# Kernel tuning notes

Measured on AMD Instinct MI355X. Metric: run time of the kernel, lower is better.

## Reference

```python
import jax, jax.numpy as jnp
import numpy as np

ENC, DEC, B, S = 1024, 1024, 32, 2048


def setup_inputs() -> dict:
    key = jax.random.key(0)
    k1, k2, k3, k4, k5, k6 = jax.random.split(key, 6)
    scale_attn = 1.0 / np.sqrt(ENC + DEC)
    return {
        "decoder_hidden": jax.random.normal(k1, (B, DEC), dtype=jnp.float32),
        "encoder_outputs": jax.random.normal(k2, (B, S, ENC), dtype=jnp.float32),
        "mask": jax.random.randint(k3, (B, S), 0, 2, dtype=jnp.int32),
        "W_attn": jax.random.normal(k4, (ENC + DEC, DEC), dtype=jnp.float32) * scale_attn,
        "b_attn": jax.random.normal(k5, (DEC,), dtype=jnp.float32) * 0.02,
        "v_w": jax.random.normal(k6, (DEC,), dtype=jnp.float32) * (1.0 / np.sqrt(DEC)),
    }


def reference(decoder_hidden, encoder_outputs, mask, W_attn, b_attn, v_w):
    # Split cat((dec_exp, enc)) @ W into two GEMMs (same math, no repeat/concat).
    dec_dim = decoder_hidden.shape[-1]
    W_dec = W_attn[:dec_dim]      # [DEC, DEC]
    W_enc = W_attn[dec_dim:]      # [ENC, DEC]
    dec_proj = decoder_hidden @ W_dec                      # [B, DEC]
    enc_proj = jnp.einsum("bse,ed->bsd", encoder_outputs, W_enc)  # [B, S, DEC]
    energy = jnp.tanh(dec_proj[:, None, :] + enc_proj + b_attn)   # [B, S, DEC]
    scores = jnp.einsum("bsd,d->bs", energy, v_w)                 # [B, S]
    scores = jnp.where(mask == 0, -1e9, scores)
    attn_weights = jax.nn.softmax(scores, axis=1)                 # [B, S]
    context = jnp.einsum("bs,bse->be", attn_weights, encoder_outputs)  # [B, ENC]
    return (context, attn_weights)
```

## Files before the change

### kernel.cpp

```cpp
#include <hip/hip_runtime.h>
#include <hip/hip_bf16.h>
#include <cstdint>


#define ENCD 1024
#define DECD 1024
#define BATCH 32
#define SEQ 2048
#define MTOT (BATCH * SEQ)
#define KDIM 1024
#define NDIM 1024

typedef __attribute__((ext_vector_type(4))) float f32x4;
typedef __attribute__((ext_vector_type(8))) __bf16 bf16x8;
typedef __attribute__((ext_vector_type(8))) unsigned short u16x8;

__device__ __forceinline__ unsigned short f2bf(float f) {
  unsigned int u = __builtin_bit_cast(unsigned int, f);
  u += 0x7fffu + ((u >> 16) & 1u);
  return (unsigned short)(u >> 16);
}

__device__ __forceinline__ float bf2f(unsigned short h) {
  return __builtin_bit_cast(float, (unsigned int)h << 16);
}

__device__ __forceinline__ void async_lds16(const unsigned short* g, unsigned short* l) {
  __builtin_amdgcn_global_load_lds(
      (const __attribute__((address_space(1))) unsigned int*)g,
      (__attribute__((address_space(3))) unsigned int*)l, 16, 0, 0);
}

__device__ __forceinline__ void barx() {
  __builtin_amdgcn_s_barrier();
  asm volatile("" ::: "memory");
}

template <int N>
__device__ __forceinline__ void waitv() {
  if constexpr (N == 0) {
    asm volatile("s_waitcnt vmcnt(0)" ::: "memory");
  } else {
    asm volatile("s_waitcnt vmcnt(8)" ::: "memory");
  }
}

__global__ void conv_bf16_k(const float* __restrict__ src, unsigned short* __restrict__ dst) {
  const long i = ((long)blockIdx.x * 256 + threadIdx.x) * 8;
  const f32x4 f0 = *(const f32x4*)(src + i);
  const f32x4 f1 = *(const f32x4*)(src + i + 4);
  u16x8 v;
  v[0] = f2bf(f0[0]); v[1] = f2bf(f0[1]); v[2] = f2bf(f0[2]); v[3] = f2bf(f0[3]);
  v[4] = f2bf(f1[0]); v[5] = f2bf(f1[1]); v[6] = f2bf(f1[2]); v[7] = f2bf(f1[3]);
  *(u16x8*)(dst + i) = v;
}

__global__ void wt_k(const float* __restrict__ W, unsigned short* __restrict__ Wt) {
  __shared__ unsigned short t[64][65];
  const int k0 = blockIdx.x * 64, n0 = blockIdx.y * 64;
  const int tx = threadIdx.x & 63, ty = threadIdx.x >> 6;
#pragma unroll
  for (int i = 0; i < 16; ++i) {
    const int k = ty + i * 4;
    t[k][tx] = f2bf(W[(long)(DECD + k0 + k) * NDIM + n0 + tx]);
  }
  __syncthreads();
#pragma unroll
  for (int i = 0; i < 16; ++i) {
    const int n = ty + i * 4;
    Wt[(long)(n0 + n) * KDIM + k0 + tx] = t[tx][n];
  }
}

__global__ __launch_bounds__(256) void prep_k(
    const float* __restrict__ dec, const float* __restrict__ enc,
    const float* __restrict__ W, const float* __restrict__ bias,
    float* __restrict__ dp, unsigned short* __restrict__ Wt,
    unsigned short* __restrict__ Abf) {
  const int gb = blockIdx.x;
  const int tid = threadIdx.x;
  if (gb < 128) {
    const int b = gb >> 2;
    const int n = (gb & 3) * 256 + tid;
    const float* d = dec + b * DECD;
    const float* w = W + n;
    float acc = bias[n];
#pragma unroll 8
    for (int k = 0; k < 1024; ++k) acc = fmaf(d[k], w[(size_t)k * NDIM], acc);
    dp[b * NDIM + n] = acc;
  } else if (gb < 384) {
    __shared__ unsigned short t[64][65];
    const int g2 = gb - 128;
    const int k0 = (g2 & 15) * 64, n0 = (g2 >> 4) * 64;
    const int tx = tid & 63, ty = tid >> 6;
#pragma unroll
    for (int i = 0; i < 16; ++i) {
      const int k = ty + i * 4;
      t[k][tx] = f2bf(W[(size_t)(DECD + k0 + k) * NDIM + n0 + tx]);
    }
    __syncthreads();
#pragma unroll
    for (int i = 0; i < 16; ++i) {
      const int n = ty + i * 4;
      Wt[(size_t)(n0 + n) * KDIM + k0 + tx] = t[tx][n];
    }
  } else {
    const long i = ((long)(gb - 384) * 256 + tid) * 8;
    const f32x4 f0 = *(const f32x4*)(enc + i);
    const f32x4 f1 = *(const f32x4*)(enc + i + 4);
    u16x8 v;
    v[0] = f2bf(f0[0]); v[1] = f2bf(f0[1]); v[2] = f2bf(f0[2]); v[3] = f2bf(f0[3]);
    v[4] = f2bf(f1[0]); v[5] = f2bf(f1[1]); v[6] = f2bf(f1[2]); v[7] = f2bf(f1[3]);
    *(u16x8*)(Abf + i) = v;
  }
}


__device__ __forceinline__ void stage4(const unsigned short* gbase, unsigned short* lbase,
                                       int wv, int srow, int schunk, int k0) {
#pragma unroll
  for (int j = 0; j < 4; ++j) {
    async_lds16(gbase + (size_t)(j * 64 + wv * 8 + srow) * KDIM + k0 + schunk * 8,
                lbase + (j * 64 + wv * 8) * 64);
  }
}

template <bool STG, int BW>
__device__ __forceinline__ void gtile2(
    unsigned short* sAc, unsigned short* sBc,
    const unsigned short* Ab, const unsigned short* Bb, int k2,
    int wm, int wn, int wv, int quad, int l15, int srow, int schunk,
    f32x4 (&acc)[8][4], bf16x8 (&aF)[4][2], bf16x8 (&bF)[4][2]) {
  const int sw = l15 & 7;
#define RDF(buf, row, h) \
  __builtin_bit_cast(bf16x8, *(const u16x8*)&(buf)[(row) * 64 + ((((h) * 4 + quad) ^ sw) * 8)])
#pragma unroll
  for (int mt = 0; mt < 4; ++mt) {
    const int row = wm * 128 + mt * 16 + l15;
    aF[mt][0] = RDF(sAc, row, 0);
    aF[mt][1] = RDF(sAc, row, 1);
  }
#pragma unroll
  for (int nt = 0; nt < 2; ++nt) {
    const int row = wn * 64 + nt * 16 + l15;
    bF[nt][0] = RDF(sBc, row, 0);
    bF[nt][1] = RDF(sBc, row, 1);
  }
  barx();
  __builtin_amdgcn_s_setprio(1);
#pragma unroll
  for (int h = 0; h < 2; ++h)
#pragma unroll
    for (int mt = 0; mt < 4; ++mt)
#pragma unroll
      for (int nt = 0; nt < 2; ++nt)
        acc[mt][nt] = __builtin_amdgcn_mfma_f32_16x16x32_bf16(aF[mt][h], bF[nt][h], acc[mt][nt], 0, 0, 0);
  __builtin_amdgcn_s_setprio(0);
  barx();
#pragma unroll
  for (int nt = 2; nt < 4; ++nt) {
    const int row = wn * 64 + nt * 16 + l15;
    bF[nt][0] = RDF(sBc, row, 0);
    bF[nt][1] = RDF(sBc, row, 1);
  }
  barx();
  __builtin_amdgcn_s_setprio(1);
#pragma unroll
  for (int h = 0; h < 2; ++h)
#pragma unroll
    for (int mt = 0; mt < 4; ++mt)
#pragma unroll
      for (int nt = 0; nt < 2; ++nt)
        acc[mt][2 + nt] = __builtin_amdgcn_mfma_f32_16x16x32_bf16(aF[mt][h], bF[2 + nt][h], acc[mt][2 + nt], 0, 0, 0);
  __builtin_amdgcn_s_setprio(0);
  barx();
#pragma unroll
  for (int mt = 0; mt < 4; ++mt) {
    const int row = wm * 128 + (4 + mt) * 16 + l15;
    aF[mt][0] = RDF(sAc, row, 0);
    aF[mt][1] = RDF(sAc, row, 1);
  }
  if (STG) stage4(Bb, sBc, wv, srow, schunk, k2);
  barx();
  __builtin_amdgcn_s_setprio(1);
#pragma unroll
  for (int h = 0; h < 2; ++h)
#pragma unroll
    for (int mt = 0; mt < 4; ++mt)
#pragma unroll
      for (int nt = 0; nt < 2; ++nt)
        acc[4 + mt][nt] = __builtin_amdgcn_mfma_f32_16x16x32_bf16(aF[mt][h], bF[nt][h], acc[4 + mt][nt], 0, 0, 0);
  __builtin_amdgcn_s_setprio(0);
  barx();
  if (STG) stage4(Ab, sAc, wv, srow, schunk, k2);
  waitv<BW>();
  barx();
  __builtin_amdgcn_s_setprio(1);
#pragma unroll
  for (int h = 0; h < 2; ++h)
#pragma unroll
    for (int mt = 0; mt < 4; ++mt)
#pragma unroll
      for (int nt = 0; nt < 2; ++nt)
        acc[4 + mt][2 + nt] = __builtin_amdgcn_mfma_f32_16x16x32_bf16(aF[mt][h], bF[2 + nt][h], acc[4 + mt][2 + nt], 0, 0, 0);
  __builtin_amdgcn_s_setprio(0);
  barx();
#undef RDF
}

__global__ __launch_bounds__(512, 2) void gemm8_k(
    const unsigned short* __restrict__ Abf, const unsigned short* __restrict__ Wt,
    const float* __restrict__ dp, const float* __restrict__ vw,
    float* __restrict__ sp) {
  __shared__ unsigned short sA[2][256 * 64];
  __shared__ unsigned short sB[2][256 * 64];
  const int tid = threadIdx.x;
  const int lane = tid & 63;
  const int wv = tid >> 6;
  const int wm = wv >> 2, wn = wv & 3;
  const int quad = lane >> 4;
  const int l15 = lane & 15;
  const int srow = lane >> 3;
  const int schunk = (lane & 7) ^ srow;

  const int f = blockIdx.x + (blockIdx.y << 2);
  const int xcd = f & 7;
  const int c = f >> 3;
  const int bn = c & 3;
  const int bm = xcd + ((c >> 2) << 3);
  const int n0 = bn * 256;
  const int row0 = bm * 256;
  const int bidx = bm >> 3;

  const unsigned short* Ab = Abf + (size_t)row0 * KDIM;
  const unsigned short* Bb = Wt + (size_t)n0 * KDIM;

  const f32x4 zz = {0.f, 0.f, 0.f, 0.f};
  f32x4 acc[8][4];
#pragma unroll
  for (int i = 0; i < 8; ++i)
#pragma unroll
    for (int j = 0; j < 4; ++j) acc[i][j] = zz;
  bf16x8 aF[4][2], bF[4][2];

  stage4(Bb, sB[0], wv, srow, schunk, 0);
  stage4(Ab, sA[0], wv, srow, schunk, 0);
  stage4(Bb, sB[1], wv, srow, schunk, 64);
  stage4(Ab, sA[1], wv, srow, schunk, 64);
  waitv<8>();
  barx();

  for (int t = 0; t < 14; t += 2) {
    gtile2<true, 8>(sA[0], sB[0], Ab, Bb, (t + 2) * 64,
                    wm, wn, wv, quad, l15, srow, schunk, acc, aF, bF);
    gtile2<true, 8>(sA[1], sB[1], Ab, Bb, (t + 3) * 64,
                    wm, wn, wv, quad, l15, srow, schunk, acc, aF, bF);
  }
  gtile2<false, 0>(sA[0], sB[0], Ab, Bb, 0,
                   wm, wn, wv, quad, l15, srow, schunk, acc, aF, bF);
  gtile2<false, 0>(sA[1], sB[1], Ab, Bb, 0,
                   wm, wn, wv, quad, l15, srow, schunk, acc, aF, bF);

  float vv[4], dv[4];
#pragma unroll
  for (int nt = 0; nt < 4; ++nt) {
    const int n = n0 + wn * 64 + nt * 16 + l15;
    vv[nt] = vw[n];
    dv[nt] = dp[bidx * NDIM + n];
  }
  float* sRed = (float*)sA;
#pragma unroll
  for (int mt = 0; mt < 8; ++mt) {
#pragma unroll
    for (int r = 0; r < 4; ++r) {
      float s = 0.f;
#pragma unroll
      for (int nt = 0; nt < 4; ++nt) {
        float x = acc[mt][nt][r] + dv[nt];
        x = fminf(fmaxf(x, -10.f), 10.f);
        const float e = __expf(2.f * x);
        s += (e - 1.f) * __builtin_amdgcn_rcpf(e + 1.f) * vv[nt];
      }
      s += __shfl_xor(s, 1);
      s += __shfl_xor(s, 2);
      s += __shfl_xor(s, 4);
      s += __shfl_xor(s, 8);
      if (l15 == 0) sRed[wn * 256 + wm * 128 + mt * 16 + quad * 4 + r] = s;
    }
  }
  __syncthreads();
  if (tid < 256) {
    const float s4 = sRed[tid] + sRed[256 + tid] + sRed[512 + tid] + sRed[768 + tid];
    sp[(size_t)bn * MTOT + row0 + tid] = s4;
  }
}

__global__ __launch_bounds__(256) void sm_ctx_k(
    const float* __restrict__ sp, const int* __restrict__ mask,
    const unsigned short* __restrict__ Abf,
    float* __restrict__ attn, float* __restrict__ ctx) {
  __shared__ float a_s[SEQ];
  __shared__ float red[16][16][8];
  __shared__ float redm[4], reds[4];
  const int ec = blockIdx.x;
  const int b = blockIdx.y;
  const int tid = threadIdx.x;
  const int w = tid >> 6;
  const int* mrow = mask + b * SEQ;
  float vals[8];
  float mx = -3.0e38f;
#pragma unroll
  for (int i = 0; i < 8; ++i) {
    const int s = tid + i * 256;
    float v = 0.f;
#pragma unroll
    for (int p = 0; p < 4; ++p) v += sp[(size_t)p * MTOT + b * SEQ + s];
    if (mrow[s] == 0) v = -1.0e9f;
    vals[i] = v;
    mx = fmaxf(mx, v);
  }
#pragma unroll
  for (int off = 1; off < 64; off <<= 1) mx = fmaxf(mx, __shfl_xor(mx, off));
  if ((tid & 63) == 0) redm[w] = mx;
  __syncthreads();
  mx = fmaxf(fmaxf(redm[0], redm[1]), fmaxf(redm[2], redm[3]));
  float sum = 0.f;
#pragma unroll
  for (int i = 0; i < 8; ++i) {
    vals[i] = __expf(vals[i] - mx);
    sum += vals[i];
  }
#pragma unroll
  for (int off = 1; off < 64; off <<= 1) sum += __shfl_xor(sum, off);
  if ((tid & 63) == 0) reds[w] = sum;
  __syncthreads();
  sum = reds[0] + reds[1] + reds[2] + reds[3];
  const float inv = 1.0f / sum;
#pragma unroll
  for (int i = 0; i < 8; ++i) {
    const float av = vals[i] * inv;
    a_s[tid + i * 256] = av;
    if (ec == 0) attn[b * SEQ + tid + i * 256] = av;
  }
  __syncthreads();
  const int sg = tid >> 4, es = tid & 15;
  const int e0 = ec * 128 + es * 8;
  const unsigned short* base = Abf + (size_t)(b * SEQ) * ENCD + e0;
  float acc[8] = {0.f, 0.f, 0.f, 0.f, 0.f, 0.f, 0.f, 0.f};
#pragma unroll 4
  for (int k = 0; k < 128; ++k) {
    const int s = sg + k * 16;
    const float wgt = a_s[s];
    const u16x8 v = *(const u16x8*)(base + (size_t)s * ENCD);
#pragma unroll
    for (int j = 0; j < 8; ++j) acc[j] = fmaf(wgt, bf2f(v[j]), acc[j]);
  }
#pragma unroll
  for (int j = 0; j < 8; ++j) red[sg][es][j] = acc[j];
  __syncthreads();
  if (tid < 128) {
    const int es2 = tid >> 3, j = tid & 7;
    float ssum = 0.f;
#pragma unroll
    for (int g = 0; g < 16; ++g) ssum += red[g][es2][j];
    ctx[b * ENCD + ec * 128 + es2 * 8 + j] = ssum;
  }
}

__global__ void dec_proj_k2(const float* __restrict__ dec, const float* __restrict__ W,
                            float* __restrict__ dp) {
  const int idx = blockIdx.x * 256 + threadIdx.x;
  const int kc = blockIdx.y;
  const int b = idx >> 10;
  const int n = idx & 1023;
  const float* d = dec + b * DECD + kc * 128;
  const float* w = W + (long)(kc * 128) * NDIM + n;
  float acc = 0.f;
#pragma unroll 8
  for (int k = 0; k < 128; ++k) acc = fmaf(d[k], w[(long)k * NDIM], acc);
  atomicAdd(&dp[idx], acc);
}

__global__ __launch_bounds__(256, 3) void gemm_scores_bf16(
    const unsigned short* __restrict__ Abf, const unsigned short* __restrict__ Wt,
    const float* __restrict__ dp, const float* __restrict__ bias,
    const float* __restrict__ vw, float* __restrict__ scores) {
  __shared__ unsigned short sA[128 * 64];
  __shared__ unsigned short sB[128 * 64];
  const int tid = threadIdx.x;
  const int lane = tid & 63;
  const int wave = tid >> 6;
  const int wm = wave >> 1, wn = wave & 1;
  const int quad = lane >> 4;
  const int l15 = lane & 15;
  const int bn = blockIdx.x, bm = blockIdx.y;
  const int n0 = bn * 128, row0 = bm * 128, bidx = bm >> 4;
  const int srow = lane >> 3;
  const int schunk = (lane & 7) ^ srow;
  const f32x4 zz = {0.f, 0.f, 0.f, 0.f};
  f32x4 acc[4][4];
#pragma unroll
  for (int i = 0; i < 4; ++i)
#pragma unroll
    for (int j = 0; j < 4; ++j) acc[i][j] = zz;
  for (int kt = 0; kt < 16; ++kt) {
    const int k0 = kt * 64;
    __syncthreads();
#pragma unroll
    for (int i = 0; i < 4; ++i) {
      const int r = wave * 32 + i * 8 + srow;
      async_lds16(Abf + (size_t)(row0 + r) * KDIM + k0 + schunk * 8,
                  &sA[(wave * 32 + i * 8) * 64]);
      async_lds16(Wt + (size_t)(n0 + r) * KDIM + k0 + schunk * 8,
                  &sB[(wave * 32 + i * 8) * 64]);
    }
    __syncthreads();
#pragma unroll
    for (int h = 0; h < 2; ++h) {
      bf16x8 af[4], bf[4];
      const int slot = ((h * 4 + quad) ^ (l15 & 7)) * 8;
#pragma unroll
      for (int t = 0; t < 4; ++t) {
        af[t] = __builtin_bit_cast(bf16x8, *(const u16x8*)&sA[(wm * 64 + t * 16 + l15) * 64 + slot]);
        bf[t] = __builtin_bit_cast(bf16x8, *(const u16x8*)&sB[(wn * 64 + t * 16 + l15) * 64 + slot]);
      }
#pragma unroll
      for (int mt = 0; mt < 4; ++mt)
#pragma unroll
        for (int nt = 0; nt < 4; ++nt)
          acc[mt][nt] = __builtin_amdgcn_mfma_f32_16x16x32_bf16(
              af[mt], bf[nt], acc[mt][nt], 0, 0, 0);
    }
  }
  float vv[4], dv[4];
#pragma unroll
  for (int nt = 0; nt < 4; ++nt) {
    const int n = n0 + wn * 64 + nt * 16 + l15;
    vv[nt] = vw[n];
    dv[nt] = dp[bidx * NDIM + n] + bias[n];
  }
#pragma unroll
  for (int mt = 0; mt < 4; ++mt) {
#pragma unroll
    for (int r = 0; r < 4; ++r) {
      float s = 0.f;
#pragma unroll
      for (int nt = 0; nt < 4; ++nt) {
        float x = acc[mt][nt][r] + dv[nt];
        x = fminf(fmaxf(x, -10.f), 10.f);
        const float e = __expf(2.f * x);
        s += (e - 1.f) * __builtin_amdgcn_rcpf(e + 1.f) * vv[nt];
      }
      s += __shfl_xor(s, 1);
      s += __shfl_xor(s, 2);
      s += __shfl_xor(s, 4);
      s += __shfl_xor(s, 8);
      if (l15 == 0) atomicAdd(&scores[row0 + wm * 64 + mt * 16 + quad * 4 + r], s);
    }
  }
}

__global__ __launch_bounds__(256, 2) void gemm_scores_f32(
    const float* __restrict__ Ag, const unsigned short* __restrict__ Wt,
    const float* __restrict__ dp, const float* __restrict__ bias,
    const float* __restrict__ vw, float* __restrict__ scores) {
  __shared__ unsigned short sA[128 * 64];
  __shared__ unsigned short sB[128 * 64];
  const int tid = threadIdx.x;
  const int lane = tid & 63;
  const int wave = tid >> 6;
  const int wm = wave >> 1, wn = wave & 1;
  const int quad = lane >> 4;
  const int l15 = lane & 15;
  const int bn = blockIdx.x, bm = blockIdx.y;
  const int n0 = bn * 128, row0 = bm * 128, bidx = bm >> 4;
  const int sr = tid >> 3, sc = tid & 7;
  const f32x4 zz = {0.f, 0.f, 0.f, 0.f};
  f32x4 acc[4][4];
#pragma unroll
  for (int i = 0; i < 4; ++i)
#pragma unroll
    for (int j = 0; j < 4; ++j) acc[i][j] = zz;
  for (int kt = 0; kt < 16; ++kt) {
    const int k0 = kt * 64;
    __syncthreads();
#pragma unroll
    for (int j = 0; j < 4; ++j) {
      const int r = sr + 32 * j;
      const int c = sc ^ (r & 7);
      const float* src = Ag + (long)(row0 + r) * KDIM + (k0 + c * 8);
      f32x4 f0 = *(const f32x4*)src;
      f32x4 f1 = *(const f32x4*)(src + 4);
      u16x8 v;
      v[0] = f2bf(f0[0]); v[1] = f2bf(f0[1]); v[2] = f2bf(f0[2]); v[3] = f2bf(f0[3]);
      v[4] = f2bf(f1[0]); v[5] = f2bf(f1[1]); v[6] = f2bf(f1[2]); v[7] = f2bf(f1[3]);
      *(u16x8*)&sA[r * 64 + sc * 8] = v;
      *(u16x8*)&sB[r * 64 + sc * 8] = *(const u16x8*)(Wt + (long)(n0 + r) * KDIM + (k0 + c * 8));
    }
    __syncthreads();
#pragma unroll
    for (int h = 0; h < 2; ++h) {
      const int cs = ((h * 4 + quad) ^ (lane & 7)) * 8;
      bf16x8 af[4], bf[4];
#pragma unroll
      for (int t = 0; t < 4; ++t) {
        af[t] = __builtin_bit_cast(bf16x8, *(const u16x8*)&sA[(wm * 64 + t * 16 + l15) * 64 + cs]);
        bf[t] = __builtin_bit_cast(bf16x8, *(const u16x8*)&sB[(wn * 64 + t * 16 + l15) * 64 + cs]);
      }
#pragma unroll
      for (int mt = 0; mt < 4; ++mt)
#pragma unroll
        for (int nt = 0; nt < 4; ++nt)
          acc[mt][nt] = __builtin_amdgcn_mfma_f32_16x16x32_bf16(
              af[mt], bf[nt], acc[mt][nt], 0, 0, 0);
    }
  }
  float vv[4], dv[4];
#pragma unroll
  for (int nt = 0; nt < 4; ++nt) {
    const int n = n0 + wn * 64 + nt * 16 + l15;
    vv[nt] = vw[n];
    dv[nt] = dp[bidx * NDIM + n] + bias[n];
  }
#pragma unroll
  for (int mt = 0; mt < 4; ++mt) {
#pragma unroll
    for (int r = 0; r < 4; ++r) {
      float s = 0.f;
#pragma unroll
      for (int nt = 0; nt < 4; ++nt) {
        float x = acc[mt][nt][r] + dv[nt];
        x = fminf(fmaxf(x, -10.f), 10.f);
        const float e = __expf(2.f * x);
        s += (e - 1.f) * __builtin_amdgcn_rcpf(e + 1.f) * vv[nt];
      }
      s += __shfl_xor(s, 1);
      s += __shfl_xor(s, 2);
      s += __shfl_xor(s, 4);
      s += __shfl_xor(s, 8);
      if (l15 == 0) atomicAdd(&scores[row0 + wm * 64 + mt * 16 + quad * 4 + r], s);
    }
  }
}

__global__ void softmax_k(float* __restrict__ sc, const int* __restrict__ mask) {
  const int b = blockIdx.x;
  const int tid = threadIdx.x;
  const int w = tid >> 6;
  __shared__ float redm[4], reds[4];
  float* row = sc + b * SEQ;
  const int* mrow = mask + b * SEQ;
  float vals[8];
  float mx = -3.0e38f;
#pragma unroll
  for (int i = 0; i < 8; ++i) {
    const int s = tid + i * 256;
    float v = row[s];
    if (mrow[s] == 0) v = -1.0e9f;
    vals[i] = v;
    mx = fmaxf(mx, v);
  }
#pragma unroll
  for (int off = 1; off < 64; off <<= 1) mx = fmaxf(mx, __shfl_xor(mx, off));
  if ((tid & 63) == 0) redm[w] = mx;
  __syncthreads();
  mx = fmaxf(fmaxf(redm[0], redm[1]), fmaxf(redm[2], redm[3]));
  float sum = 0.f;
#pragma unroll
  for (int i = 0; i < 8; ++i) {
    vals[i] = __expf(vals[i] - mx);
    sum += vals[i];
  }
#pragma unroll
  for (int off = 1; off < 64; off <<= 1) sum += __shfl_xor(sum, off);
  if ((tid & 63) == 0) reds[w] = sum;
  __syncthreads();
  sum = reds[0] + reds[1] + reds[2] + reds[3];
  const float inv = 1.0f / sum;
#pragma unroll
  for (int i = 0; i < 8; ++i) row[tid + i * 256] = vals[i] * inv;
}

__global__ void context_k(const float* __restrict__ attn, const float* __restrict__ enc,
                          float* __restrict__ ctx) {
  const int b = blockIdx.y;
  const int s0 = blockIdx.x * 32;
  const int e = threadIdx.x * 4;
  const float* arow = attn + b * SEQ + s0;
  const float* ebase = enc + (long)(b * SEQ + s0) * ENCD + e;
  f32x4 acc = {0.f, 0.f, 0.f, 0.f};
#pragma unroll 8
  for (int s = 0; s < 32; ++s) {
    const float w = arow[s];
    const f32x4 v = *(const f32x4*)(ebase + (long)s * ENCD);
    acc += w * v;
  }
  float* dst = ctx + b * ENCD + e;
  atomicAdd(dst + 0, acc[0]);
  atomicAdd(dst + 1, acc[1]);
  atomicAdd(dst + 2, acc[2]);
  atomicAdd(dst + 3, acc[3]);
}

extern "C" void kernel_launch(void* const* d_in, const int* in_sizes, int n_in,
                              void* d_out, int out_size, void* d_ws, size_t ws_size,
                              hipStream_t stream) {
  (void)in_sizes; (void)n_in; (void)out_size;
  const float* dec  = (const float*)d_in[0];
  const float* enc  = (const float*)d_in[1];
  const int*   mask = (const int*)d_in[2];
  const float* W    = (const float*)d_in[3];
  const float* bias = (const float*)d_in[4];
  const float* vw   = (const float*)d_in[5];

  float* ctx  = (float*)d_out;
  float* attn = (float*)d_out + BATCH * ENCD;
  unsigned short* Wt  = (unsigned short*)d_ws;
  unsigned short* Abf = (unsigned short*)((char*)d_ws + (2ull << 20));
  float* shared = (float*)((char*)d_ws + (130ull << 20));

  const size_t needA = (132ull << 20);
  const size_t needB = (2ull << 20) + ((size_t)MTOT * KDIM * 2);

  if (ws_size >= needA) {
    prep_k<<<384 + 32768, 256, 0, stream>>>(dec, enc, W, bias, ctx, Wt, Abf);
    gemm8_k<<<dim3(4, 256), 512, 0, stream>>>(Abf, Wt, ctx, vw, shared);
    sm_ctx_k<<<dim3(8, 32), 256, 0, stream>>>(shared, mask, Abf, attn, ctx);
  } else if (ws_size >= needB) {
    wt_k<<<dim3(16, 16), 256, 0, stream>>>(W, Wt);
    hipMemsetAsync(attn, 0, (size_t)MTOT * sizeof(float), stream);
    hipMemsetAsync(ctx, 0, (size_t)(BATCH * NDIM) * sizeof(float), stream);
    dec_proj_k2<<<dim3(128, 8), 256, 0, stream>>>(dec, W, ctx);
    conv_bf16_k<<<32768, 256, 0, stream>>>(enc, Abf);
    gemm_scores_bf16<<<dim3(8, 512), 256, 0, stream>>>(Abf, Wt, ctx, bias, vw, attn);
    softmax_k<<<32, 256, 0, stream>>>(attn, mask);
    hipMemsetAsync(ctx, 0, (size_t)(BATCH * ENCD) * sizeof(float), stream);
    context_k<<<dim3(64, 32), 256, 0, stream>>>(attn, enc, ctx);
  } else {
    wt_k<<<dim3(16, 16), 256, 0, stream>>>(W, Wt);
    hipMemsetAsync(attn, 0, (size_t)MTOT * sizeof(float), stream);
    hipMemsetAsync(ctx, 0, (size_t)(BATCH * NDIM) * sizeof(float), stream);
    dec_proj_k2<<<dim3(128, 8), 256, 0, stream>>>(dec, W, ctx);
    gemm_scores_f32<<<dim3(8, 512), 256, 0, stream>>>(enc, Wt, ctx, bias, vw, attn);
    softmax_k<<<32, 256, 0, stream>>>(attn, mask);
    hipMemsetAsync(ctx, 0, (size_t)(BATCH * ENCD) * sizeof(float), stream);
    context_k<<<dim3(64, 32), 256, 0, stream>>>(attn, enc, ctx);
  }
}
```

Baseline: 584.5 us.

## Register double-buffer MFMA fragments across K tiles with fewer barriers

Replaces the four-phase per-tile schedule, which reloaded fragments in halves between barriers, with a loop that reads a whole tile's A/B fragments into a second register set. That read overlaps the full 64-MFMA block on the current set. Global-to-LDS staging is now issued at the start of each half-iteration, and there are fewer barriers per tile. The aim is to hide LDS read latency behind MFMAs and cut synchronisation overhead. The cost is much higher VGPR pressure from two full fragment sets plus the accumulators, which risks spills or lower occupancy under the 512x2 launch bounds.

```diff
diff --git a/kernel.cpp b/kernel.cpp
--- a/kernel.cpp
+++ b/kernel.cpp
@@ -43,6 +43,11 @@
   } else {
     asm volatile("s_waitcnt vmcnt(8)" ::: "memory");
   }
+}
+
+__device__ __forceinline__ void waitlgkm0() {
+  asm volatile("s_waitcnt lgkmcnt(0)" ::: "memory");
+  __builtin_amdgcn_sched_barrier(0);
 }
 
 __global__ void conv_bf16_k(const float* __restrict__ src, unsigned short* __restrict__ dst) {
@@ -125,87 +130,40 @@
   }
 }
 
-template <bool STG, int BW>
-__device__ __forceinline__ void gtile2(
-    unsigned short* sAc, unsigned short* sBc,
-    const unsigned short* Ab, const unsigned short* Bb, int k2,
-    int wm, int wn, int wv, int quad, int l15, int srow, int schunk,
-    f32x4 (&acc)[8][4], bf16x8 (&aF)[4][2], bf16x8 (&bF)[4][2]) {
+__device__ __forceinline__ void rdfrags(const unsigned short* sAc, const unsigned short* sBc,
+                                        int wm, int wn, int quad, int l15,
+                                        bf16x8 (&a)[8][2], bf16x8 (&b)[4][2]) {
   const int sw = l15 & 7;
-#define RDF(buf, row, h) \
-  __builtin_bit_cast(bf16x8, *(const u16x8*)&(buf)[(row) * 64 + ((((h) * 4 + quad) ^ sw) * 8)])
-#pragma unroll
-  for (int mt = 0; mt < 4; ++mt) {
+#pragma unroll
+  for (int mt = 0; mt < 8; ++mt) {
     const int row = wm * 128 + mt * 16 + l15;
-    aF[mt][0] = RDF(sAc, row, 0);
-    aF[mt][1] = RDF(sAc, row, 1);
-  }
-#pragma unroll
-  for (int nt = 0; nt < 2; ++nt) {
+#pragma unroll
+    for (int h = 0; h < 2; ++h)
+      a[mt][h] = __builtin_bit_cast(bf16x8,
+          *(const u16x8*)&sAc[row * 64 + (((h * 4 + quad) ^ sw) * 8)]);
+  }
+#pragma unroll
+  for (int nt = 0; nt < 4; ++nt) {
     const int row = wn * 64 + nt * 16 + l15;
-    bF[nt][0] = RDF(sBc, row, 0);
-    bF[nt][1] = RDF(sBc, row, 1);
-  }
-  barx();
+#pragma unroll
+    for (int h = 0; h < 2; ++h)
+      b[nt][h] = __builtin_bit_cast(bf16x8,
+          *(const u16x8*)&sBc[row * 64 + (((h * 4 + quad) ^ sw) * 8)]);
+  }
+}
+
+__device__ __forceinline__ void mfma64(f32x4 (&acc)[8][4],
+                                       const bf16x8 (&a)[8][2], const bf16x8 (&b)[4][2]) {
   __builtin_amdgcn_s_setprio(1);
 #pragma unroll
   for (int h = 0; h < 2; ++h)
 #pragma unroll
-    for (int mt = 0; mt < 4; ++mt)
-#pragma unroll
-      for (int nt = 0; nt < 2; ++nt)
-        acc[mt][nt] = __builtin_amdgcn_mfma_f32_16x16x32_bf16(aF[mt][h], bF[nt][h], acc[mt][nt], 0, 0, 0);
+    for (int mt = 0; mt < 8; ++mt)
+#pragma unroll
+      for (int nt = 0; nt < 4; ++nt)
+        acc[mt][nt] = __builtin_amdgcn_mfma_f32_16x16x32_bf16(
+            a[mt][h], b[nt][h], acc[mt][nt], 0, 0, 0);
   __builtin_amdgcn_s_setprio(0);
-  barx();
-#pragma unroll
-  for (int nt = 2; nt < 4; ++nt) {
-    const int row = wn * 64 + nt * 16 + l15;
-    bF[nt][0] = RDF(sBc, row, 0);
-    bF[nt][1] = RDF(sBc, row, 1);
-  }
-  barx();
-  __builtin_amdgcn_s_setprio(1);
-#pragma unroll
-  for (int h = 0; h < 2; ++h)
-#pragma unroll
-    for (int mt = 0; mt < 4; ++mt)
-#pragma unroll
-      for (int nt = 0; nt < 2; ++nt)
-        acc[mt][2 + nt] = __builtin_amdgcn_mfma_f32_16x16x32_bf16(aF[mt][h], bF[2 + nt][h], acc[mt][2 + nt], 0, 0, 0);
-  __builtin_amdgcn_s_setprio(0);
-  barx();
-#pragma unroll
-  for (int mt = 0; mt < 4; ++mt) {
-    const int row = wm * 128 + (4 + mt) * 16 + l15;
-    aF[mt][0] = RDF(sAc, row, 0);
-    aF[mt][1] = RDF(sAc, row, 1);
-  }
-  if (STG) stage4(Bb, sBc, wv, srow, schunk, k2);
-  barx();
-  __builtin_amdgcn_s_setprio(1);
-#pragma unroll
-  for (int h = 0; h < 2; ++h)
-#pragma unroll
-    for (int mt = 0; mt < 4; ++mt)
-#pragma unroll
-      for (int nt = 0; nt < 2; ++nt)
-        acc[4 + mt][nt] = __builtin_amdgcn_mfma_f32_16x16x32_bf16(aF[mt][h], bF[nt][h], acc[4 + mt][nt], 0, 0, 0);
-  __builtin_amdgcn_s_setprio(0);
-  barx();
-  if (STG) stage4(Ab, sAc, wv, srow, schunk, k2);
-  waitv<BW>();
-  barx();
-  __builtin_amdgcn_s_setprio(1);
-#pragma unroll
-  for (int h = 0; h < 2; ++h)
-#pragma unroll
-    for (int mt = 0; mt < 4; ++mt)
-#pragma unroll
-      for (int nt = 0; nt < 2; ++nt)
-        acc[4 + mt][2 + nt] = __builtin_amdgcn_mfma_f32_16x16x32_bf16(aF[mt][h], bF[2 + nt][h], acc[4 + mt][2 + nt], 0, 0, 0);
-  __builtin_amdgcn_s_setprio(0);
-  barx();
-#undef RDF
 }
 
 __global__ __launch_bounds__(512, 2) void gemm8_k(
@@ -241,7 +199,8 @@
   for (int i = 0; i < 8; ++i)
 #pragma unroll
     for (int j = 0; j < 4; ++j) acc[i][j] = zz;
-  bf16x8 aF[4][2], bF[4][2];
+  bf16x8 aC[8][2], bC[4][2];
+  bf16x8 aN[8][2], bN[4][2];
 
   stage4(Bb, sB[0], wv, srow, schunk, 0);
   stage4(Ab, sA[0], wv, srow, schunk, 0);
@@ -249,17 +208,39 @@
   stage4(Ab, sA[1], wv, srow, schunk, 64);
   waitv<8>();
   barx();
-
-  for (int t = 0; t < 14; t += 2) {
-    gtile2<true, 8>(sA[0], sB[0], Ab, Bb, (t + 2) * 64,
-                    wm, wn, wv, quad, l15, srow, schunk, acc, aF, bF);
-    gtile2<true, 8>(sA[1], sB[1], Ab, Bb, (t + 3) * 64,
-                    wm, wn, wv, quad, l15, srow, schunk, acc, aF, bF);
-  }
-  gtile2<false, 0>(sA[0], sB[0], Ab, Bb, 0,
-                   wm, wn, wv, quad, l15, srow, schunk, acc, aF, bF);
-  gtile2<false, 0>(sA[1], sB[1], Ab, Bb, 0,
-                   wm, wn, wv, quad, l15, srow, schunk, acc, aF, bF);
+  rdfrags(sA[0], sB[0], wm, wn, quad, l15, aC, bC);
+  waitlgkm0();
+  barx();
+
+#pragma unroll 1
+  for (int pr = 0; pr < 7; ++pr) {
+    const int t = pr * 2;
+    stage4(Bb, sB[0], wv, srow, schunk, (t + 2) * 64);
+    stage4(Ab, sA[0], wv, srow, schunk, (t + 2) * 64);
+    waitv<8>();
+    barx();
+    rdfrags(sA[1], sB[1], wm, wn, quad, l15, aN, bN);
+    __builtin_amdgcn_sched_barrier(0);
+    mfma64(acc, aC, bC);
+    waitlgkm0();
+    barx();
+    stage4(Bb, sB[1], wv, srow, schunk, (t + 3) * 64);
+    stage4(Ab, sA[1], wv, srow, schunk, (t + 3) * 64);
+    waitv<8>();
+    barx();
+    rdfrags(sA[0], sB[0], wm, wn, quad, l15, aC, bC);
+    __builtin_amdgcn_sched_barrier(0);
+    mfma64(acc, aN, bN);
+    waitlgkm0();
+    barx();
+  }
+  waitv<0>();
+  barx();
+  rdfrags(sA[1], sB[1], wm, wn, quad, l15, aN, bN);
+  __builtin_amdgcn_sched_barrier(0);
+  mfma64(acc, aC, bC);
+  waitlgkm0();
+  mfma64(acc, aN, bN);
 
   float vv[4], dv[4];
 #pragma unroll
```

After: 1.374 ms. +135.0%, slower.
